# Optimization experiments

Hardware: AMD Instinct MI355X
Metric: run time of the kernel (lower is better)

Reference implementation:

```python
import jax, jax.numpy as jnp
import numpy as np

B, N, D, H, HID = 8, 729, 1152, 12, 4304
HD = D // H
EPS = 1e-6


def _layer_norm(x, g, b):
    mu = jnp.mean(x, axis=-1, keepdims=True)
    var = jnp.mean((x - mu) ** 2, axis=-1, keepdims=True)
    return (x - mu) / jnp.sqrt(var + EPS) * g + b


def setup_inputs() -> dict:
    key = jax.random.key(0)
    ks = jax.random.split(key, 9)
    s = 0.02
    return {
        "x": jax.random.normal(ks[0], (B, N, D), jnp.float32),
        "wq": jax.random.normal(ks[1], (D, D), jnp.float32) * s,
        "bq": jnp.zeros((D,), jnp.float32),
        "wk": jax.random.normal(ks[2], (D, D), jnp.float32) * s,
        "bk": jnp.zeros((D,), jnp.float32),
        "wv": jax.random.normal(ks[3], (D, D), jnp.float32) * s,
        "bv": jnp.zeros((D,), jnp.float32),
        "wo": jax.random.normal(ks[4], (D, D), jnp.float32) * s,
        "bo": jnp.zeros((D,), jnp.float32),
        "ln1_g": jnp.ones((D,), jnp.float32),
        "ln1_b": jnp.zeros((D,), jnp.float32),
        "w_fc1": jax.random.normal(ks[5], (HID, D), jnp.float32) * s,
        "b_fc1": jnp.zeros((HID,), jnp.float32),
        "w_fc2": jax.random.normal(ks[6], (D, HID), jnp.float32) * s,
        "b_fc2": jnp.zeros((D,), jnp.float32),
        "ln2_g": jnp.ones((D,), jnp.float32),
        "ln2_b": jnp.zeros((D,), jnp.float32),
    }


def reference(x, wq, bq, wk, bk, wv, bv, wo, bo, ln1_g, ln1_b,
              w_fc1, b_fc1, w_fc2, b_fc2, ln2_g, ln2_b):
    b, n, d = x.shape
    # split_heads in the source is a plain view (B, H, N, HD) -- NOT a transpose.
    def heads(t):
        return t.reshape(b, H, n, HD)

    Q = heads(x @ wq.T + bq)
    K = heads(x @ wk.T + bk)
    V = heads(x @ wv.T + bv)

    scores = jnp.einsum("bhqd,bhkd->bhqk", Q, K) * (HD ** -0.5)
    attn_w = jax.nn.softmax(scores, axis=-1)
    o = jnp.einsum("bhqk,bhkd->bhqd", attn_w, V)  # [B,H,N,HD]
    o = jnp.swapaxes(o, 1, 2).reshape(b, n, d)
    attn_out = o @ wo.T + bo

    # post-norm: LN(sublayer) + residual
    h = _layer_norm(attn_out, ln1_g, ln1_b) + x

    # quirky MLP: activation applied BEFORE fc1 (faithful to source)
    m = jax.nn.gelu(h, approximate=True)
    m = m @ w_fc1.T + b_fc1
    m = m @ w_fc2.T + b_fc2

    return _layer_norm(m, ln2_g, ln2_b) + h
```

## Files before the change

### kernel.cpp

```cpp
#include <hip/hip_runtime.h>
#include <hip/hip_bf16.h>

#define BF16 __hip_bfloat16

typedef short short8 __attribute__((ext_vector_type(8)));
typedef short short4v __attribute__((ext_vector_type(4)));
typedef float v4f __attribute__((ext_vector_type(4)));
typedef float f4 __attribute__((ext_vector_type(4)));

__device__ __forceinline__ short f2bs(float f) {
    __hip_bfloat16 h = __float2bfloat16(f);
    return *(short*)&h;
}

__device__ __forceinline__ float bs2f(short s) {
    __hip_bfloat16 h = *(__hip_bfloat16*)&s;
    return __bfloat162float(h);
}

__device__ __forceinline__ void async_cp16(const BF16* g, BF16* l) {
    __builtin_amdgcn_global_load_lds(
        (const __attribute__((address_space(1))) void*)g,
        (__attribute__((address_space(3))) void*)l,
        16, 0, 0);
}

__global__ __launch_bounds__(256) void cvt_all_kernel(
    const float* __restrict__ wq, const float* __restrict__ wk,
    const float* __restrict__ wv, const float* __restrict__ wo,
    const float* __restrict__ wfc2, const float* __restrict__ x,
    BF16* __restrict__ wbq, BF16* __restrict__ wbk,
    BF16* __restrict__ wbv, BF16* __restrict__ wbo,
    BF16* __restrict__ wbf2, BF16* __restrict__ xb)
{
    const int i = blockIdx.x * 256 + threadIdx.x;
    constexpr int N_DD  = 331776;
    constexpr int N4    = 4 * N_DD;
    constexpr int N_F2  = 1253376;
    constexpr int E_F2  = N4 + N_F2;
    constexpr int N_X   = 1679616;
    constexpr int TOTAL = E_F2 + N_X;

    if (i < N4) {
        int seg = i / N_DD, j = i - seg * N_DD;
        const float* s = (seg == 0) ? wq : (seg == 1) ? wk : (seg == 2) ? wv : wo;
        BF16* d = (seg == 0) ? wbq : (seg == 1) ? wbk : (seg == 2) ? wbv : wbo;
        f4 v = ((const f4*)s)[j];
        short4v o = {f2bs(v.x), f2bs(v.y), f2bs(v.z), f2bs(v.w)};
        ((short4v*)d)[j] = o;
    } else if (i < E_F2) {
        int j = i - N4;
        int row = j / 1088;
        int c = (j - row * 1088) * 4;
        short4v o = {0, 0, 0, 0};
        if (c < 4304) {
            f4 v = *(const f4*)(wfc2 + (size_t)row * 4304 + c);
            o[0] = f2bs(v.x); o[1] = f2bs(v.y); o[2] = f2bs(v.z); o[3] = f2bs(v.w);
        }
        *(short4v*)(wbf2 + (size_t)row * 4352 + c) = o;
    } else if (i < TOTAL) {
        int j = i - E_F2;
        f4 v = ((const f4*)x)[j];
        short4v o = {f2bs(v.x), f2bs(v.y), f2bs(v.z), f2bs(v.w)};
        ((short4v*)xb)[j] = o;
    }
}

__global__ __launch_bounds__(256) void w1t_kernel(
    const float* __restrict__ wfc1, BF16* __restrict__ w1t)
{
    __shared__ float tile[64][65];
    const int h0 = blockIdx.x * 64;
    const int d0 = blockIdx.y * 64;
    const int tid = threadIdx.x;
#pragma unroll
    for (int i = 0; i < 4; ++i) {
        int lin = tid + i * 256;
        int r = lin >> 4, c4 = lin & 15;
        f4 v = {0.f, 0.f, 0.f, 0.f};
        if (h0 + r < 4304)
            v = *(const f4*)(wfc1 + (size_t)(h0 + r) * 1152 + d0 + c4 * 4);
        tile[r][c4 * 4 + 0] = v.x;
        tile[r][c4 * 4 + 1] = v.y;
        tile[r][c4 * 4 + 2] = v.z;
        tile[r][c4 * 4 + 3] = v.w;
    }
    __syncthreads();
#pragma unroll
    for (int i = 0; i < 2; ++i) {
        int lin = tid + i * 256;
        int dr = lin >> 3, h8 = lin & 7;
        short8 o;
#pragma unroll
        for (int e = 0; e < 8; ++e)
            o[e] = f2bs(tile[h8 * 8 + e][dr]);
        *(short8*)(w1t + (size_t)(d0 + dr) * 4352 + h0 + h8 * 8) = o;
    }
}

__global__ __launch_bounds__(256) void bias_fuse_kernel(
    const float* __restrict__ wfc2, const float* __restrict__ bfc1,
    const float* __restrict__ bfc2, float* __restrict__ bp)
{
    const int row = blockIdx.x * 4 + (threadIdx.x >> 6);
    const int lane = threadIdx.x & 63;
    const float* wr = wfc2 + (size_t)row * 4304;
    float s = 0.f;
    for (int k = lane; k < 4304; k += 64) s += wr[k] * bfc1[k];
#pragma unroll
    for (int mm = 1; mm < 64; mm <<= 1) s += __shfl_xor(s, mm, 64);
    if (lane == 0) bp[row] = s + bfc2[row];
}

__global__ __launch_bounds__(256) void transpose_v3(
    const BF16* __restrict__ V, BF16* __restrict__ VT)
{
    const int hg = blockIdx.x;
    const int s  = blockIdx.y;
    const int b = hg / 12, hh = hg - b * 12;
    const BF16* src = V + (size_t)b * (729 * 1152) + (size_t)hh * (729 * 96);
    BF16* dst = VT + (size_t)hg * 112 * 768;
    const BF16 z = __float2bfloat16(0.f);
    const BF16 one = __float2bfloat16(1.f);
    for (int hd = s * 28; hd < s * 28 + 28; ++hd) {
        for (int kk = threadIdx.x; kk < 768; kk += 256) {
            BF16 val;
            if (hd < 96)       val = (kk < 729) ? src[(size_t)kk * 96 + hd] : z;
            else if (hd == 96) val = (kk < 729) ? one : z;
            else               val = z;
            dst[(size_t)hd * 768 + kk] = val;
        }
    }
}

template<int TM>
__global__ __launch_bounds__(256) void gemm_bt_t(
    const BF16* __restrict__ A, int lda,
    const BF16* __restrict__ W, int ldb,
    const float* __restrict__ bias, int nbias,
    BF16* __restrict__ C, int ldc,
    int M, int Kr)
{
    constexpr int MT = TM / 32;
    __shared__ __align__(16) BF16 smem[(TM + 128) * 64];
    BF16* As = smem;
    BF16* Bs = smem + TM * 64;

    const int tid  = threadIdx.x;
    const int lane = tid & 63;
    const int wave = tid >> 6;
    const int quad = lane >> 4;
    const int l16  = lane & 15;
    const int wm   = (wave >> 1) * (TM / 2);
    const int wn   = (wave & 1) * 64;
    const int m0   = blockIdx.x * TM;
    const int n0   = blockIdx.y * 128;
    if (m0 >= M) return;

    const v4f zf = {0.f, 0.f, 0.f, 0.f};
    v4f acc[MT][4];
#pragma unroll
    for (int i = 0; i < MT; ++i)
#pragma unroll
        for (int j = 0; j < 4; ++j) acc[i][j] = zf;

    const BF16* gA[MT]; BF16* lA[MT];
#pragma unroll
    for (int i = 0; i < MT; ++i) {
        int c = tid + i * 256;
        gA[i] = A + (size_t)(m0 + (c >> 3)) * lda + ((((c & 7) - (c >> 3)) & 7) << 3);
        lA[i] = As + (c & ~63) * 8;
    }
    const BF16* gB[4]; BF16* lB[4];
#pragma unroll
    for (int i = 0; i < 4; ++i) {
        int c = tid + i * 256;
        gB[i] = W + (size_t)(n0 + (c >> 3)) * ldb + ((((c & 7) - (c >> 3)) & 7) << 3);
        lB[i] = Bs + (c & ~63) * 8;
    }

    const int nk = Kr >> 6;
    for (int kt = 0; kt < nk; ++kt) {
#pragma unroll
        for (int i = 0; i < MT; ++i) { async_cp16(gA[i], lA[i]); gA[i] += 64; }
#pragma unroll
        for (int i = 0; i < 4; ++i)  { async_cp16(gB[i], lB[i]); gB[i] += 64; }
        __syncthreads();

#pragma unroll
        for (int ks = 0; ks < 2; ++ks) {
            short8 af[MT], bfg[4];
#pragma unroll
            for (int mt = 0; mt < MT; ++mt) {
                int row = wm + mt * 16 + l16;
                af[mt] = *(const short8*)(As + row * 64 + ((((ks << 2) | quad) + row & 7) & 7) * 8);
            }
#pragma unroll
            for (int nt = 0; nt < 4; ++nt) {
                int row = wn + nt * 16 + l16;
                bfg[nt] = *(const short8*)(Bs + row * 64 + ((((ks << 2) | quad) + row & 7) & 7) * 8);
            }
#pragma unroll
            for (int mt = 0; mt < MT; ++mt)
#pragma unroll
                for (int nt = 0; nt < 4; ++nt)
                    acc[mt][nt] = __builtin_amdgcn_mfma_f32_16x16x32_bf16(
                        af[mt], bfg[nt], acc[mt][nt], 0, 0, 0);
        }
        __syncthreads();
    }

    float bv[4];
#pragma unroll
    for (int nt = 0; nt < 4; ++nt) {
        int col = n0 + wn + nt * 16 + l16;
        bv[nt] = (col < nbias) ? bias[col] : 0.f;
    }
#pragma unroll
    for (int mt = 0; mt < MT; ++mt)
#pragma unroll
        for (int nt = 0; nt < 4; ++nt)
#pragma unroll
            for (int r2 = 0; r2 < 4; ++r2) {
                int row_l = wm + mt * 16 + quad * 4 + r2;
                int col_l = wn + nt * 16 + l16;
                smem[row_l * 128 + col_l] = __float2bfloat16(acc[mt][nt][r2] + bv[nt]);
            }
    __syncthreads();
#pragma unroll
    for (int p = 0; p < TM / 16; ++p) {
        int idx = p * 256 + tid;
        int row = m0 + (idx >> 4);
        if (row < M)
            *(short8*)(C + (size_t)row * ldc + n0 + (idx & 15) * 8) =
                *(const short8*)(smem + idx * 8);
    }
}

__global__ __launch_bounds__(256) void gemm_merge_splitk(
    const BF16* __restrict__ A,
    const BF16* __restrict__ W,
    float* __restrict__ P)
{
    constexpr int TM = 64, MT = 2;
    __shared__ __align__(16) BF16 smem[(TM + 128) * 64];
    BF16* As = smem;
    BF16* Bs = smem + TM * 64;

    const int tid  = threadIdx.x;
    const int lane = tid & 63;
    const int wave = tid >> 6;
    const int quad = lane >> 4;
    const int l16  = lane & 15;
    const int wm   = (wave >> 1) * 32;
    const int wn   = (wave & 1) * 64;
    const int m0   = blockIdx.x * TM;
    const int n0   = blockIdx.y * 128;
    const int z    = blockIdx.z;
    const int ks0  = (z < 4) ? 9 * z : 36 + 8 * (z - 4);
    const int nk   = (z < 4) ? 9 : 8;

    const v4f zf = {0.f, 0.f, 0.f, 0.f};
    v4f acc[MT][4];
#pragma unroll
    for (int i = 0; i < MT; ++i)
#pragma unroll
        for (int j = 0; j < 4; ++j) acc[i][j] = zf;

    const BF16* gA[MT]; BF16* lA[MT];
#pragma unroll
    for (int i = 0; i < MT; ++i) {
        int c = tid + i * 256;
        gA[i] = A + (size_t)(m0 + (c >> 3)) * 4352 + ((((c & 7) - (c >> 3)) & 7) << 3)
              + ks0 * 64;
        lA[i] = As + (c & ~63) * 8;
    }
    const BF16* gB[4]; BF16* lB[4];
#pragma unroll
    for (int i = 0; i < 4; ++i) {
        int c = tid + i * 256;
        gB[i] = W + (size_t)(n0 + (c >> 3)) * 4352 + ((((c & 7) - (c >> 3)) & 7) << 3)
              + ks0 * 64;
        lB[i] = Bs + (c & ~63) * 8;
    }

    for (int kt = 0; kt < nk; ++kt) {
#pragma unroll
        for (int i = 0; i < MT; ++i) { async_cp16(gA[i], lA[i]); gA[i] += 64; }
#pragma unroll
        for (int i = 0; i < 4; ++i)  { async_cp16(gB[i], lB[i]); gB[i] += 64; }
        __syncthreads();

#pragma unroll
        for (int ks = 0; ks < 2; ++ks) {
            short8 af[MT], bfg[4];
#pragma unroll
            for (int mt = 0; mt < MT; ++mt) {
                int row = wm + mt * 16 + l16;
                af[mt] = *(const short8*)(As + row * 64 + ((((ks << 2) | quad) + row & 7) & 7) * 8);
            }
#pragma unroll
            for (int nt = 0; nt < 4; ++nt) {
                int row = wn + nt * 16 + l16;
                bfg[nt] = *(const short8*)(Bs + row * 64 + ((((ks << 2) | quad) + row & 7) & 7) * 8);
            }
#pragma unroll
            for (int mt = 0; mt < MT; ++mt)
#pragma unroll
                for (int nt = 0; nt < 4; ++nt)
                    acc[mt][nt] = __builtin_amdgcn_mfma_f32_16x16x32_bf16(
                        af[mt], bfg[nt], acc[mt][nt], 0, 0, 0);
        }
        __syncthreads();
    }

    float* Pz = P + (size_t)z * 1327104;
#pragma unroll
    for (int mt = 0; mt < MT; ++mt)
#pragma unroll
        for (int nt = 0; nt < 4; ++nt)
#pragma unroll
            for (int r2 = 0; r2 < 4; ++r2) {
                int row = m0 + wm + mt * 16 + quad * 4 + r2;
                int col = n0 + wn + nt * 16 + l16;
                Pz[(size_t)row * 1152 + col] = acc[mt][nt][r2];
            }
}

__global__ __launch_bounds__(256) void wm_reduce_kernel(
    const float* __restrict__ P, BF16* __restrict__ Wm)
{
    const int i = blockIdx.x * 256 + threadIdx.x;
    f4 s = ((const f4*)P)[i];
#pragma unroll
    for (int z = 1; z < 8; ++z) {
        f4 v = ((const f4*)(P + (size_t)z * 1327104))[i];
        s.x += v.x; s.y += v.y; s.z += v.z; s.w += v.w;
    }
    short4v o = {f2bs(s.x), f2bs(s.y), f2bs(s.z), f2bs(s.w)};
    ((short4v*)Wm)[i] = o;
}

__global__ __launch_bounds__(256) void gemm_qkv(
    const BF16* __restrict__ A,
    const BF16* __restrict__ W,
    const float* __restrict__ b0, const float* __restrict__ b1,
    const float* __restrict__ b2,
    BF16* __restrict__ C, size_t cstride, int M)
{
    __shared__ __align__(16) BF16 smem[256 * 64];
    BF16* As = smem;
    BF16* Bs = smem + 128 * 64;

    const int tid  = threadIdx.x;
    const int lane = tid & 63;
    const int wave = tid >> 6;
    const int quad = lane >> 4;
    const int l16  = lane & 15;
    const int wm   = (wave >> 1) * 64;
    const int wn   = (wave & 1) * 64;
    const int m0   = blockIdx.x * 128;
    const int n0   = blockIdx.y * 128;
    if (m0 >= M) return;

    const v4f zf = {0.f, 0.f, 0.f, 0.f};
    v4f acc[4][4];
#pragma unroll
    for (int i = 0; i < 4; ++i)
#pragma unroll
        for (int j = 0; j < 4; ++j) acc[i][j] = zf;

    const BF16* gA[4]; BF16* lA[4];
    const BF16* gB[4]; BF16* lB[4];
#pragma unroll
    for (int i = 0; i < 4; ++i) {
        int c = tid + i * 256;
        int src = ((((c & 7) - (c >> 3)) & 7) << 3);
        gA[i] = A + (size_t)(m0 + (c >> 3)) * 1152 + src;
        gB[i] = W + (size_t)(n0 + (c >> 3)) * 1152 + src;
        lA[i] = As + (c & ~63) * 8;
        lB[i] = Bs + (c & ~63) * 8;
    }

    for (int kt = 0; kt < 18; ++kt) {
#pragma unroll
        for (int i = 0; i < 4; ++i) { async_cp16(gA[i], lA[i]); gA[i] += 64; }
#pragma unroll
        for (int i = 0; i < 4; ++i) { async_cp16(gB[i], lB[i]); gB[i] += 64; }
        __syncthreads();

#pragma unroll
        for (int ks = 0; ks < 2; ++ks) {
            short8 af[4], bfg[4];
#pragma unroll
            for (int mt = 0; mt < 4; ++mt) {
                int row = wm + mt * 16 + l16;
                af[mt] = *(const short8*)(As + row * 64 + ((((ks << 2) | quad) + row & 7) & 7) * 8);
            }
#pragma unroll
            for (int nt = 0; nt < 4; ++nt) {
                int row = wn + nt * 16 + l16;
                bfg[nt] = *(const short8*)(Bs + row * 64 + ((((ks << 2) | quad) + row & 7) & 7) * 8);
            }
#pragma unroll
            for (int mt = 0; mt < 4; ++mt)
#pragma unroll
                for (int nt = 0; nt < 4; ++nt)
                    acc[mt][nt] = __builtin_amdgcn_mfma_f32_16x16x32_bf16(
                        af[mt], bfg[nt], acc[mt][nt], 0, 0, 0);
        }
        __syncthreads();
    }

    const int sel = n0 / 1152;
    const float* bp = (sel == 0) ? b0 : (sel == 1) ? b1 : b2;
    BF16* Cb = C + (size_t)sel * cstride;
    const int nl0 = n0 - sel * 1152;

    float bv[4];
#pragma unroll
    for (int nt = 0; nt < 4; ++nt)
        bv[nt] = bp[nl0 + wn + nt * 16 + l16];
#pragma unroll
    for (int mt = 0; mt < 4; ++mt)
#pragma unroll
        for (int nt = 0; nt < 4; ++nt)
#pragma unroll
            for (int r2 = 0; r2 < 4; ++r2) {
                int row_l = wm + mt * 16 + quad * 4 + r2;
                int col_l = wn + nt * 16 + l16;
                smem[row_l * 128 + col_l] = __float2bfloat16(acc[mt][nt][r2] + bv[nt]);
            }
    __syncthreads();
#pragma unroll
    for (int p = 0; p < 8; ++p) {
        int idx = p * 256 + tid;
        int row = m0 + (idx >> 4);
        if (row < M)
            *(short8*)(Cb + (size_t)row * 1152 + nl0 + (idx & 15) * 8) =
                *(const short8*)(smem + idx * 8);
    }
}

__global__ __launch_bounds__(256) void attn_flash3(
    const BF16* __restrict__ Q, const BF16* __restrict__ K,
    const BF16* __restrict__ VT, BF16* __restrict__ O)
{
    constexpr int NQ = 729, HDk = 96, DM = 1152, LDV = 768;
    __shared__ __align__(16) BF16 Ks[64 * 104];
    __shared__ __align__(16) BF16 Vs[112 * 64];
    __shared__ __align__(16) BF16 Ps[4][32 * 72];

    const int id = blockIdx.x;
    const int xcd = id & 7, slot = id >> 3;
    const int hb = slot / 6, qt = slot - hb * 6;
    const int hg = xcd * 12 + hb;
    const int b = hg / 12, hh = hg - b * 12;

    const int tid = threadIdx.x, wave = tid >> 6, lane = tid & 63;
    const int quad = lane >> 4, l16 = lane & 15;
    const size_t kbase = (size_t)b * (NQ * DM) + (size_t)hh * (NQ * HDk);
    const size_t vbase = (size_t)hg * 112 * LDV;

    const short8 zero8 = {0, 0, 0, 0, 0, 0, 0, 0};
    const v4f zf = {0.f, 0.f, 0.f, 0.f};
    const float C2 = 0.14724445f;

    const int q0w = qt * 128 + wave * 32;
    short8 aq[2][3];
#pragma unroll
    for (int mt = 0; mt < 2; ++mt) {
        int qrow = q0w + mt * 16 + l16;
#pragma unroll
        for (int ks = 0; ks < 3; ++ks)
            aq[mt][ks] = (qrow < NQ)
                ? *(const short8*)(Q + kbase + (size_t)qrow * HDk + ks * 32 + quad * 8)
                : zero8;
    }

    int kk_[3], kg_[3];
#pragma unroll
    for (int i = 0; i < 3; ++i) {
        int c = tid + i * 256;
        kk_[i] = c / 12; kg_[i] = c - kk_[i] * 12;
    }
    int vq_[4], vgr_[4], vhd_[4];
#pragma unroll
    for (int i = 0; i < 4; ++i) {
        int q = wave + 4 * i;
        vq_[i] = q;
        int hd = q * 8 + (lane >> 3);
        vhd_[i] = hd;
        vgr_[i] = ((lane & 7) - hd) & 7;
    }

    v4f oacc[2][7];
#pragma unroll
    for (int mt = 0; mt < 2; ++mt)
#pragma unroll
        for (int nt = 0; nt < 7; ++nt) oacc[mt][nt] = zf;

    for (int kt = 0; kt < 12; ++kt) {
        const int k0 = kt * 64;
#pragma unroll
        for (int i = 0; i < 4; ++i) {
            if (vq_[i] < 14)
                async_cp16(VT + vbase + (size_t)vhd_[i] * LDV + k0 + vgr_[i] * 8,
                           Vs + vq_[i] * 512);
        }
#pragma unroll
        for (int i = 0; i < 3; ++i) {
            short8 v = *(const short8*)(K + kbase + (size_t)(k0 + kk_[i]) * HDk + kg_[i] * 8);
            *(short8*)(Ks + kk_[i] * 104 + kg_[i] * 8) = v;
        }
        __syncthreads();

        v4f s[2][4];
#pragma unroll
        for (int mt = 0; mt < 2; ++mt)
#pragma unroll
            for (int nt = 0; nt < 4; ++nt) s[mt][nt] = zf;
#pragma unroll
        for (int ks = 0; ks < 3; ++ks)
#pragma unroll
            for (int nt = 0; nt < 4; ++nt) {
                short8 bk = *(const short8*)(Ks + (nt * 16 + l16) * 104 + ks * 32 + quad * 8);
#pragma unroll
                for (int mt = 0; mt < 2; ++mt)
                    s[mt][nt] = __builtin_amdgcn_mfma_f32_16x16x32_bf16(
                        aq[mt][ks], bk, s[mt][nt], 0, 0, 0);
            }

        BF16* Pw = &Ps[wave][0];
#pragma unroll
        for (int mt = 0; mt < 2; ++mt)
#pragma unroll
            for (int nt = 0; nt < 4; ++nt)
#pragma unroll
                for (int r = 0; r < 4; ++r)
                    Pw[(mt * 16 + quad * 4 + r) * 72 + nt * 16 + l16] =
                        __float2bfloat16(exp2f(s[mt][nt][r] * C2));
        asm volatile("s_waitcnt lgkmcnt(0)" ::: "memory");

        short8 ap[2][2];
#pragma unroll
        for (int mt = 0; mt < 2; ++mt)
#pragma unroll
            for (int kc = 0; kc < 2; ++kc)
                ap[mt][kc] = *(const short8*)(Pw + (mt * 16 + l16) * 72 + kc * 32 + quad * 8);
#pragma unroll
        for (int nt = 0; nt < 7; ++nt) {
            int hd = nt * 16 + l16;
#pragma unroll
            for (int kc = 0; kc < 2; ++kc) {
                short8 bv = *(const short8*)(Vs + hd * 64 + (((kc * 4 + quad) + hd & 7) & 7) * 8);
#pragma unroll
                for (int mt = 0; mt < 2; ++mt)
                    oacc[mt][nt] = __builtin_amdgcn_mfma_f32_16x16x32_bf16(
                        ap[mt][kc], bv, oacc[mt][nt], 0, 0, 0);
            }
        }
        __syncthreads();
    }

#pragma unroll
    for (int mt = 0; mt < 2; ++mt) {
        const int qb = q0w + mt * 16 + quad * 4;
#pragma unroll
        for (int r = 0; r < 4; ++r) {
            int q = qb + r;
            float lv = __shfl(oacc[mt][6][r], quad << 4, 64);
            float inv = (lv > 0.f) ? 1.f / lv : 0.f;
            if (q >= NQ) continue;
#pragma unroll
            for (int nt = 0; nt < 6; ++nt)
                O[(size_t)b * (NQ * DM) + (size_t)q * DM + hh * HDk + nt * 16 + l16] =
                    __float2bfloat16(oacc[mt][nt][r] * inv);
        }
    }
}

__device__ __forceinline__ float block_sum256(float v, float* red, int tid)
{
#pragma unroll
    for (int mm = 1; mm < 64; mm <<= 1) v += __shfl_xor(v, mm, 64);
    if ((tid & 63) == 0) red[tid >> 6] = v;
    __syncthreads();
    float r = red[0] + red[1] + red[2] + red[3];
    __syncthreads();
    return r;
}

__global__ __launch_bounds__(256) void ln1_gelu_kernel(
    const BF16* __restrict__ ao, const float* __restrict__ x,
    const float* __restrict__ gw, const float* __restrict__ bw,
    BF16* __restrict__ hout, BF16* __restrict__ gout)
{
    __shared__ float red[4];
    const int row = blockIdx.x, tid = threadIdx.x;
    const bool act = tid < 144;
    float v[8];
    float s = 0.f;
    if (act) {
        short8 pk = ((const short8*)(ao + (size_t)row * 1152))[tid];
#pragma unroll
        for (int j = 0; j < 8; ++j) { v[j] = bs2f(pk[j]); s += v[j]; }
    } else {
#pragma unroll
        for (int j = 0; j < 8; ++j) v[j] = 0.f;
    }
    s = block_sum256(s, red, tid);
    float mu = s * (1.f / 1152.f);
    float vsum = 0.f;
    if (act) {
#pragma unroll
        for (int j = 0; j < 8; ++j) { float d = v[j] - mu; vsum += d * d; }
    }
    vsum = block_sum256(vsum, red, tid);
    float rstd = rsqrtf(vsum * (1.f / 1152.f) + 1e-6f);
    if (act) {
        f4 g0 = ((const f4*)gw)[2 * tid], g1 = ((const f4*)gw)[2 * tid + 1];
        f4 b0 = ((const f4*)bw)[2 * tid], b1 = ((const f4*)bw)[2 * tid + 1];
        const f4* xr = (const f4*)(x + (size_t)row * 1152);
        f4 x0 = xr[2 * tid], x1 = xr[2 * tid + 1];
        short8 ho, go;
#pragma unroll
        for (int j = 0; j < 8; ++j) {
            float gj = (j < 4) ? g0[j] : g1[j - 4];
            float bj = (j < 4) ? b0[j] : b1[j - 4];
            float xj = (j < 4) ? x0[j] : x1[j - 4];
            float hv = (v[j] - mu) * rstd * gj + bj + xj;
            ho[j] = f2bs(hv);
            float t = hv;
            float gl = 0.5f * t * (1.f + tanhf(0.7978845608028654f * (t + 0.044715f * t * t * t)));
            go[j] = f2bs(gl);
        }
        ((short8*)(hout + (size_t)row * 1152))[tid] = ho;
        ((short8*)(gout + (size_t)row * 1152))[tid] = go;
    }
}

__global__ __launch_bounds__(256) void ln2_kernel(
    const BF16* __restrict__ m2, const BF16* __restrict__ hf,
    const float* __restrict__ gw, const float* __restrict__ bw,
    float* __restrict__ out)
{
    __shared__ float red[4];
    const int row = blockIdx.x, tid = threadIdx.x;
    const bool act = tid < 144;
    float v[8];
    float s = 0.f;
    if (act) {
        short8 pk = ((const short8*)(m2 + (size_t)row * 1152))[tid];
#pragma unroll
        for (int j = 0; j < 8; ++j) { v[j] = bs2f(pk[j]); s += v[j]; }
    } else {
#pragma unroll
        for (int j = 0; j < 8; ++j) v[j] = 0.f;
    }
    s = block_sum256(s, red, tid);
    float mu = s * (1.f / 1152.f);
    float vsum = 0.f;
    if (act) {
#pragma unroll
        for (int j = 0; j < 8; ++j) { float d = v[j] - mu; vsum += d * d; }
    }
    vsum = block_sum256(vsum, red, tid);
    float rstd = rsqrtf(vsum * (1.f / 1152.f) + 1e-6f);
    if (act) {
        f4 g0 = ((const f4*)gw)[2 * tid], g1 = ((const f4*)gw)[2 * tid + 1];
        f4 b0 = ((const f4*)bw)[2 * tid], b1 = ((const f4*)bw)[2 * tid + 1];
        short8 hfv = ((const short8*)(hf + (size_t)row * 1152))[tid];
        f4 o0, o1;
#pragma unroll
        for (int j = 0; j < 8; ++j) {
            float gj = (j < 4) ? g0[j] : g1[j - 4];
            float bj = (j < 4) ? b0[j] : b1[j - 4];
            float ov = (v[j] - mu) * rstd * gj + bj + bs2f(hfv[j]);
            if (j < 4) o0[j] = ov; else o1[j - 4] = ov;
        }
        f4* orow = (f4*)(out + (size_t)row * 1152);
        orow[2 * tid] = o0;
        orow[2 * tid + 1] = o1;
    }
}

extern "C" void kernel_launch(void* const* d_in, const int* in_sizes, int n_in,
                              void* d_out, int out_size, void* d_ws, size_t ws_size,
                              hipStream_t stream)
{
    const float* x    = (const float*)d_in[0];
    const float* wq   = (const float*)d_in[1];
    const float* bq   = (const float*)d_in[2];
    const float* wk   = (const float*)d_in[3];
    const float* bk   = (const float*)d_in[4];
    const float* wv   = (const float*)d_in[5];
    const float* bv   = (const float*)d_in[6];
    const float* wo   = (const float*)d_in[7];
    const float* bo   = (const float*)d_in[8];
    const float* ln1g = (const float*)d_in[9];
    const float* ln1b = (const float*)d_in[10];
    const float* wfc1 = (const float*)d_in[11];
    const float* bfc1 = (const float*)d_in[12];
    const float* wfc2 = (const float*)d_in[13];
    const float* bfc2 = (const float*)d_in[14];
    const float* ln2g = (const float*)d_in[15];
    const float* ln2b = (const float*)d_in[16];

    const int T = 8 * 729;
    const int D = 1152, HIDP = 4352;
    const size_t TD = (size_t)T * D;
    const size_t WDD = (size_t)D * D;

    BF16* wbq   = (BF16*)d_ws;
    BF16* wbk   = wbq + WDD;
    BF16* wbv   = wbk + WDD;
    BF16* wbo   = wbv + WDD;
    BF16* wbf1t = wbo + WDD;
    BF16* wbf2  = wbf1t + (size_t)HIDP * D;
    BF16* xb    = wbf2 + (size_t)D * HIDP;
    BF16* S0    = xb + TD;
    BF16* S1    = S0 + TD;
    BF16* S2    = S1 + TD;
    BF16* S3    = S2 + TD;
    BF16* C0    = S3 + TD;
    BF16* C1    = C0 + TD;
    BF16* VT    = C0;
    float* Pws  = (float*)S0;
    BF16* Wm    = xb;
    float* bp   = (float*)(xb + WDD + WDD);

    dim3 blk(256);

    cvt_all_kernel<<<16641, blk, 0, stream>>>(
        wq, wk, wv, wo, wfc2, x, wbq, wbk, wbv, wbo, wbf2, xb);

    gemm_qkv<<<dim3(46, 27), blk, 0, stream>>>(xb, wbq, bq, bk, bv, S0, TD, T);

    transpose_v3<<<dim3(96, 4), blk, 0, stream>>>(S2, VT);
    attn_flash3<<<576, blk, 0, stream>>>(S0, S1, VT, S3);

    gemm_bt_t<64><<<dim3(92, 9), blk, 0, stream>>>(S3, D, wbo, D, bo, D, C0, D, T, D);

    ln1_gelu_kernel<<<T, blk, 0, stream>>>(C0, x, ln1g, ln1b, C1, C0);

    w1t_kernel<<<dim3(68, 18), blk, 0, stream>>>(wfc1, wbf1t);
    bias_fuse_kernel<<<288, blk, 0, stream>>>(wfc2, bfc1, bfc2, bp);
    gemm_merge_splitk<<<dim3(18, 9, 8), blk, 0, stream>>>(wbf2, wbf1t, Pws);
    wm_reduce_kernel<<<1296, blk, 0, stream>>>(Pws, Wm);
    gemm_bt_t<64><<<dim3(92, 9), blk, 0, stream>>>(C0, D, Wm, D, bp, D, S3, D, T, D);

    ln2_kernel<<<T, blk, 0, stream>>>(S3, C1, ln2g, ln2b, (float*)d_out);
}
```

Before: 447.3 us.

## Fuse prep kernels and co-schedule weight-merge GEMM with QKV GEMM

Merges the conversion, fc1 transpose and bias-fuse kernels into one launch, and runs the fc2·fc1 weight-merge split-K GEMM (now 2-way split instead of 8) in the same grid as the QKV projection. It also fuses the V transpose, rewritten with a tiled LDS swizzle and vectorised stores, with the split-K reduction. The fused bias now lives in a device global. The aim is fewer launches, better CU fill from concurrent heterogeneous blocks, and less partial-sum traffic. The cost is longer per-block K loops in the merge GEMM and branchy heterogeneous kernels.

```diff
diff --git a/kernel.cpp b/kernel.cpp
--- a/kernel.cpp
+++ b/kernel.cpp
@@ -7,6 +7,8 @@
 typedef short short4v __attribute__((ext_vector_type(4)));
 typedef float v4f __attribute__((ext_vector_type(4)));
 typedef float f4 __attribute__((ext_vector_type(4)));
+
+__device__ float g_bp[1152];
 
 __device__ __forceinline__ short f2bs(float f) {
     __hip_bfloat16 h = __float2bfloat16(f);
@@ -25,111 +27,323 @@
         16, 0, 0);
 }
 
-__global__ __launch_bounds__(256) void cvt_all_kernel(
+__global__ __launch_bounds__(256) void prep_kernel(
     const float* __restrict__ wq, const float* __restrict__ wk,
     const float* __restrict__ wv, const float* __restrict__ wo,
-    const float* __restrict__ wfc2, const float* __restrict__ x,
+    const float* __restrict__ wfc1, const float* __restrict__ wfc2,
+    const float* __restrict__ x,
+    const float* __restrict__ bfc1, const float* __restrict__ bfc2,
     BF16* __restrict__ wbq, BF16* __restrict__ wbk,
     BF16* __restrict__ wbv, BF16* __restrict__ wbo,
-    BF16* __restrict__ wbf2, BF16* __restrict__ xb)
-{
-    const int i = blockIdx.x * 256 + threadIdx.x;
-    constexpr int N_DD  = 331776;
-    constexpr int N4    = 4 * N_DD;
-    constexpr int N_F2  = 1253376;
-    constexpr int E_F2  = N4 + N_F2;
-    constexpr int N_X   = 1679616;
-    constexpr int TOTAL = E_F2 + N_X;
-
-    if (i < N4) {
-        int seg = i / N_DD, j = i - seg * N_DD;
-        const float* s = (seg == 0) ? wq : (seg == 1) ? wk : (seg == 2) ? wv : wo;
-        BF16* d = (seg == 0) ? wbq : (seg == 1) ? wbk : (seg == 2) ? wbv : wbo;
-        f4 v = ((const f4*)s)[j];
-        short4v o = {f2bs(v.x), f2bs(v.y), f2bs(v.z), f2bs(v.w)};
-        ((short4v*)d)[j] = o;
-    } else if (i < E_F2) {
-        int j = i - N4;
-        int row = j / 1088;
-        int c = (j - row * 1088) * 4;
-        short4v o = {0, 0, 0, 0};
-        if (c < 4304) {
-            f4 v = *(const f4*)(wfc2 + (size_t)row * 4304 + c);
-            o[0] = f2bs(v.x); o[1] = f2bs(v.y); o[2] = f2bs(v.z); o[3] = f2bs(v.w);
-        }
-        *(short4v*)(wbf2 + (size_t)row * 4352 + c) = o;
-    } else if (i < TOTAL) {
-        int j = i - E_F2;
-        f4 v = ((const f4*)x)[j];
-        short4v o = {f2bs(v.x), f2bs(v.y), f2bs(v.z), f2bs(v.w)};
-        ((short4v*)xb)[j] = o;
-    }
-}
-
-__global__ __launch_bounds__(256) void w1t_kernel(
-    const float* __restrict__ wfc1, BF16* __restrict__ w1t)
+    BF16* __restrict__ wbf1t, BF16* __restrict__ wbf2,
+    BF16* __restrict__ xb)
 {
     __shared__ float tile[64][65];
-    const int h0 = blockIdx.x * 64;
-    const int d0 = blockIdx.y * 64;
+    const int bid = blockIdx.x;
     const int tid = threadIdx.x;
-#pragma unroll
-    for (int i = 0; i < 4; ++i) {
-        int lin = tid + i * 256;
-        int r = lin >> 4, c4 = lin & 15;
-        f4 v = {0.f, 0.f, 0.f, 0.f};
-        if (h0 + r < 4304)
-            v = *(const f4*)(wfc1 + (size_t)(h0 + r) * 1152 + d0 + c4 * 4);
-        tile[r][c4 * 4 + 0] = v.x;
-        tile[r][c4 * 4 + 1] = v.y;
-        tile[r][c4 * 4 + 2] = v.z;
-        tile[r][c4 * 4 + 3] = v.w;
-    }
-    __syncthreads();
-#pragma unroll
-    for (int i = 0; i < 2; ++i) {
-        int lin = tid + i * 256;
-        int dr = lin >> 3, h8 = lin & 7;
-        short8 o;
-#pragma unroll
-        for (int e = 0; e < 8; ++e)
-            o[e] = f2bs(tile[h8 * 8 + e][dr]);
-        *(short8*)(w1t + (size_t)(d0 + dr) * 4352 + h0 + h8 * 8) = o;
-    }
-}
-
-__global__ __launch_bounds__(256) void bias_fuse_kernel(
-    const float* __restrict__ wfc2, const float* __restrict__ bfc1,
-    const float* __restrict__ bfc2, float* __restrict__ bp)
-{
-    const int row = blockIdx.x * 4 + (threadIdx.x >> 6);
-    const int lane = threadIdx.x & 63;
-    const float* wr = wfc2 + (size_t)row * 4304;
-    float s = 0.f;
-    for (int k = lane; k < 4304; k += 64) s += wr[k] * bfc1[k];
-#pragma unroll
-    for (int mm = 1; mm < 64; mm <<= 1) s += __shfl_xor(s, mm, 64);
-    if (lane == 0) bp[row] = s + bfc2[row];
-}
-
-__global__ __launch_bounds__(256) void transpose_v3(
-    const BF16* __restrict__ V, BF16* __restrict__ VT)
-{
-    const int hg = blockIdx.x;
-    const int s  = blockIdx.y;
-    const int b = hg / 12, hh = hg - b * 12;
-    const BF16* src = V + (size_t)b * (729 * 1152) + (size_t)hh * (729 * 96);
-    BF16* dst = VT + (size_t)hg * 112 * 768;
-    const BF16 z = __float2bfloat16(0.f);
-    const BF16 one = __float2bfloat16(1.f);
-    for (int hd = s * 28; hd < s * 28 + 28; ++hd) {
-        for (int kk = threadIdx.x; kk < 768; kk += 256) {
-            BF16 val;
-            if (hd < 96)       val = (kk < 729) ? src[(size_t)kk * 96 + hd] : z;
-            else if (hd == 96) val = (kk < 729) ? one : z;
-            else               val = z;
-            dst[(size_t)hd * 768 + kk] = val;
-        }
+
+    if (bid < 16641) {
+        const int i = bid * 256 + tid;
+        constexpr int N_DD  = 331776;
+        constexpr int N4    = 4 * N_DD;
+        constexpr int N_F2  = 1253376;
+        constexpr int E_F2  = N4 + N_F2;
+        constexpr int N_X   = 1679616;
+        constexpr int TOTAL = E_F2 + N_X;
+
+        if (i < N4) {
+            int seg = i / N_DD, j = i - seg * N_DD;
+            const float* s = (seg == 0) ? wq : (seg == 1) ? wk : (seg == 2) ? wv : wo;
+            BF16* d = (seg == 0) ? wbq : (seg == 1) ? wbk : (seg == 2) ? wbv : wbo;
+            f4 v = ((const f4*)s)[j];
+            short4v o = {f2bs(v.x), f2bs(v.y), f2bs(v.z), f2bs(v.w)};
+            ((short4v*)d)[j] = o;
+        } else if (i < E_F2) {
+            int j = i - N4;
+            int row = j / 1088;
+            int c = (j - row * 1088) * 4;
+            short4v o = {0, 0, 0, 0};
+            if (c < 4304) {
+                f4 v = *(const f4*)(wfc2 + (size_t)row * 4304 + c);
+                o[0] = f2bs(v.x); o[1] = f2bs(v.y); o[2] = f2bs(v.z); o[3] = f2bs(v.w);
+            }
+            *(short4v*)(wbf2 + (size_t)row * 4352 + c) = o;
+        } else if (i < TOTAL) {
+            int j = i - E_F2;
+            f4 v = ((const f4*)x)[j];
+            short4v o = {f2bs(v.x), f2bs(v.y), f2bs(v.z), f2bs(v.w)};
+            ((short4v*)xb)[j] = o;
+        }
+    } else if (bid < 17865) {
+        const int b2 = bid - 16641;
+        const int h0 = (b2 % 68) * 64;
+        const int d0 = (b2 / 68) * 64;
+#pragma unroll
+        for (int i = 0; i < 4; ++i) {
+            int lin = tid + i * 256;
+            int r = lin >> 4, c4 = lin & 15;
+            f4 v = {0.f, 0.f, 0.f, 0.f};
+            if (h0 + r < 4304)
+                v = *(const f4*)(wfc1 + (size_t)(h0 + r) * 1152 + d0 + c4 * 4);
+            tile[r][c4 * 4 + 0] = v.x;
+            tile[r][c4 * 4 + 1] = v.y;
+            tile[r][c4 * 4 + 2] = v.z;
+            tile[r][c4 * 4 + 3] = v.w;
+        }
+        __syncthreads();
+#pragma unroll
+        for (int i = 0; i < 2; ++i) {
+            int lin = tid + i * 256;
+            int dr = lin >> 3, h8 = lin & 7;
+            short8 o;
+#pragma unroll
+            for (int e = 0; e < 8; ++e)
+                o[e] = f2bs(tile[h8 * 8 + e][dr]);
+            *(short8*)(wbf1t + (size_t)(d0 + dr) * 4352 + h0 + h8 * 8) = o;
+        }
+    } else {
+        const int row = (bid - 17865) * 4 + (tid >> 6);
+        const int lane = tid & 63;
+        const float* wr = wfc2 + (size_t)row * 4304;
+        float s = 0.f;
+        for (int k = lane; k < 4304; k += 64) s += wr[k] * bfc1[k];
+#pragma unroll
+        for (int mm = 1; mm < 64; mm <<= 1) s += __shfl_xor(s, mm, 64);
+        if (lane == 0) g_bp[row] = s + bfc2[row];
+    }
+}
+
+__global__ __launch_bounds__(256) void qkv_merge_kernel(
+    const BF16* __restrict__ A,
+    const BF16* __restrict__ Wqkv,
+    const float* __restrict__ b0, const float* __restrict__ b1,
+    const float* __restrict__ b2,
+    BF16* __restrict__ C, size_t cstride, int M,
+    const BF16* __restrict__ W2,
+    const BF16* __restrict__ W1t,
+    float* __restrict__ P)
+{
+    __shared__ __align__(16) BF16 smem[256 * 64];
+    const int bid  = blockIdx.x;
+    const int tid  = threadIdx.x;
+    const int lane = tid & 63;
+    const int wave = tid >> 6;
+    const int quad = lane >> 4;
+    const int l16  = lane & 15;
+    const v4f zf = {0.f, 0.f, 0.f, 0.f};
+
+    if (bid < 324) {
+        BF16* As = smem;
+        BF16* Bs = smem + 64 * 64;
+        const int mx = bid % 18, ny = (bid / 18) % 9, z = bid / 162;
+        const int m0 = mx * 64, n0 = ny * 128;
+        const int ks0 = z * 34;
+        const int wm = (wave >> 1) * 32;
+        const int wn = (wave & 1) * 64;
+
+        v4f acc[2][4];
+#pragma unroll
+        for (int i = 0; i < 2; ++i)
+#pragma unroll
+            for (int j = 0; j < 4; ++j) acc[i][j] = zf;
+
+        const BF16* gA[2]; BF16* lA[2];
+#pragma unroll
+        for (int i = 0; i < 2; ++i) {
+            int c = tid + i * 256;
+            gA[i] = W2 + (size_t)(m0 + (c >> 3)) * 4352 + ((((c & 7) - (c >> 3)) & 7) << 3)
+                  + ks0 * 64;
+            lA[i] = As + (c & ~63) * 8;
+        }
+        const BF16* gB[4]; BF16* lB[4];
+#pragma unroll
+        for (int i = 0; i < 4; ++i) {
+            int c = tid + i * 256;
+            gB[i] = W1t + (size_t)(n0 + (c >> 3)) * 4352 + ((((c & 7) - (c >> 3)) & 7) << 3)
+                  + ks0 * 64;
+            lB[i] = Bs + (c & ~63) * 8;
+        }
+
+        for (int kt = 0; kt < 34; ++kt) {
+#pragma unroll
+            for (int i = 0; i < 2; ++i) { async_cp16(gA[i], lA[i]); gA[i] += 64; }
+#pragma unroll
+            for (int i = 0; i < 4; ++i)  { async_cp16(gB[i], lB[i]); gB[i] += 64; }
+            __syncthreads();
+#pragma unroll
+            for (int ks = 0; ks < 2; ++ks) {
+                short8 af[2], bfg[4];
+#pragma unroll
+                for (int mt = 0; mt < 2; ++mt) {
+                    int row = wm + mt * 16 + l16;
+                    af[mt] = *(const short8*)(As + row * 64 + ((((ks << 2) | quad) + row & 7) & 7) * 8);
+                }
+#pragma unroll
+                for (int nt = 0; nt < 4; ++nt) {
+                    int row = wn + nt * 16 + l16;
+                    bfg[nt] = *(const short8*)(Bs + row * 64 + ((((ks << 2) | quad) + row & 7) & 7) * 8);
+                }
+#pragma unroll
+                for (int mt = 0; mt < 2; ++mt)
+#pragma unroll
+                    for (int nt = 0; nt < 4; ++nt)
+                        acc[mt][nt] = __builtin_amdgcn_mfma_f32_16x16x32_bf16(
+                            af[mt], bfg[nt], acc[mt][nt], 0, 0, 0);
+            }
+            __syncthreads();
+        }
+
+        float* Pz = P + (size_t)z * 1327104;
+#pragma unroll
+        for (int mt = 0; mt < 2; ++mt)
+#pragma unroll
+            for (int nt = 0; nt < 4; ++nt)
+#pragma unroll
+                for (int r2 = 0; r2 < 4; ++r2) {
+                    int row = m0 + wm + mt * 16 + quad * 4 + r2;
+                    int col = n0 + wn + nt * 16 + l16;
+                    Pz[(size_t)row * 1152 + col] = acc[mt][nt][r2];
+                }
+    } else {
+        BF16* As = smem;
+        BF16* Bs = smem + 128 * 64;
+        const int id2 = bid - 324;
+        const int m0 = (id2 % 46) * 128;
+        const int n0 = (id2 / 46) * 128;
+        const int wm = (wave >> 1) * 64;
+        const int wn = (wave & 1) * 64;
+
+        v4f acc[4][4];
+#pragma unroll
+        for (int i = 0; i < 4; ++i)
+#pragma unroll
+            for (int j = 0; j < 4; ++j) acc[i][j] = zf;
+
+        const BF16* gA[4]; BF16* lA[4];
+        const BF16* gB[4]; BF16* lB[4];
+#pragma unroll
+        for (int i = 0; i < 4; ++i) {
+            int c = tid + i * 256;
+            int src = ((((c & 7) - (c >> 3)) & 7) << 3);
+            gA[i] = A + (size_t)(m0 + (c >> 3)) * 1152 + src;
+            gB[i] = Wqkv + (size_t)(n0 + (c >> 3)) * 1152 + src;
+            lA[i] = As + (c & ~63) * 8;
+            lB[i] = Bs + (c & ~63) * 8;
+        }
+
+        for (int kt = 0; kt < 18; ++kt) {
+#pragma unroll
+            for (int i = 0; i < 4; ++i) { async_cp16(gA[i], lA[i]); gA[i] += 64; }
+#pragma unroll
+            for (int i = 0; i < 4; ++i) { async_cp16(gB[i], lB[i]); gB[i] += 64; }
+            __syncthreads();
+#pragma unroll
+            for (int ks = 0; ks < 2; ++ks) {
+                short8 af[4], bfg[4];
+#pragma unroll
+                for (int mt = 0; mt < 4; ++mt) {
+                    int row = wm + mt * 16 + l16;
+                    af[mt] = *(const short8*)(As + row * 64 + ((((ks << 2) | quad) + row & 7) & 7) * 8);
+                }
+#pragma unroll
+                for (int nt = 0; nt < 4; ++nt) {
+                    int row = wn + nt * 16 + l16;
+                    bfg[nt] = *(const short8*)(Bs + row * 64 + ((((ks << 2) | quad) + row & 7) & 7) * 8);
+                }
+#pragma unroll
+                for (int mt = 0; mt < 4; ++mt)
+#pragma unroll
+                    for (int nt = 0; nt < 4; ++nt)
+                        acc[mt][nt] = __builtin_amdgcn_mfma_f32_16x16x32_bf16(
+                            af[mt], bfg[nt], acc[mt][nt], 0, 0, 0);
+            }
+            __syncthreads();
+        }
+
+        const int sel = n0 / 1152;
+        const float* bp = (sel == 0) ? b0 : (sel == 1) ? b1 : b2;
+        BF16* Cb = C + (size_t)sel * cstride;
+        const int nl0 = n0 - sel * 1152;
+
+        float bv[4];
+#pragma unroll
+        for (int nt = 0; nt < 4; ++nt)
+            bv[nt] = bp[nl0 + wn + nt * 16 + l16];
+#pragma unroll
+        for (int mt = 0; mt < 4; ++mt)
+#pragma unroll
+            for (int nt = 0; nt < 4; ++nt)
+#pragma unroll
+                for (int r2 = 0; r2 < 4; ++r2) {
+                    int row_l = wm + mt * 16 + quad * 4 + r2;
+                    int col_l = wn + nt * 16 + l16;
+                    smem[row_l * 128 + col_l] = __float2bfloat16(acc[mt][nt][r2] + bv[nt]);
+                }
+        __syncthreads();
+#pragma unroll
+        for (int p = 0; p < 8; ++p) {
+            int idx = p * 256 + tid;
+            int row = m0 + (idx >> 4);
+            if (row < M)
+                *(short8*)(Cb + (size_t)row * 1152 + nl0 + (idx & 15) * 8) =
+                    *(const short8*)(smem + idx * 8);
+        }
+    }
+}
+
+__global__ __launch_bounds__(256) void trans_reduce_kernel(
+    const BF16* __restrict__ V, BF16* __restrict__ VT,
+    const float* __restrict__ P, BF16* __restrict__ Wm)
+{
+    __shared__ __align__(16) BF16 tl[64][128];
+    const int bid = blockIdx.x, tid = threadIdx.x;
+    const short8 zero8 = {0, 0, 0, 0, 0, 0, 0, 0};
+
+    if (bid < 1152) {
+        const int hg = bid / 12, kb = bid - hg * 12;
+        const int b = hg / 12, hh = hg - b * 12;
+        const BF16* src = V + (size_t)b * 839808 + (size_t)hh * 69984;
+        BF16* dst = VT + (size_t)hg * 86016;
+        const int kk0 = kb * 64;
+#pragma unroll
+        for (int i = 0; i < 3; ++i) {
+            int c = tid + i * 256;
+            int r = c / 12, cg = c - r * 12;
+            short8 v = (kk0 + r < 729)
+                ? *(const short8*)(src + (size_t)(kk0 + r) * 96 + cg * 8) : zero8;
+            *(short8*)(&tl[r][(cg ^ ((r >> 3) & 7)) * 8]) = v;
+        }
+        __syncthreads();
+#pragma unroll
+        for (int i = 0; i < 3; ++i) {
+            int wc = tid + i * 256;
+            int hd = wc >> 3, o = wc & 7;
+            int sp = (((hd >> 3) ^ o) << 3) + (hd & 7);
+            short8 out;
+#pragma unroll
+            for (int j = 0; j < 8; ++j)
+                out[j] = *(const short*)&tl[o * 8 + j][sp];
+            *(short8*)(dst + (size_t)hd * 768 + kk0 + o * 8) = out;
+        }
+    } else if (bid < 1728) {
+        int c = (bid - 1152) * 256 + tid;
+        int hg = c / 1536, rem = c - hg * 1536;
+        int r = rem / 96, ock = rem - r * 96;
+        int kk = ock * 8;
+        short8 v = zero8;
+        if (r == 0) {
+            const short oneb = 0x3F80;
+#pragma unroll
+            for (int j = 0; j < 8; ++j) v[j] = (kk + j < 729) ? oneb : (short)0;
+        }
+        *(short8*)(VT + (size_t)hg * 86016 + (size_t)(96 + r) * 768 + kk) = v;
+    } else {
+        int i = (bid - 1728) * 256 + tid;
+        f4 s = ((const f4*)P)[i];
+        f4 v = ((const f4*)(P + 1327104))[i];
+        s.x += v.x; s.y += v.y; s.z += v.z; s.w += v.w;
+        short4v o = {f2bs(s.x), f2bs(s.y), f2bs(s.z), f2bs(s.w)};
+        ((short4v*)Wm)[i] = o;
     }
 }
 
@@ -233,211 +447,6 @@
         int row = m0 + (idx >> 4);
         if (row < M)
             *(short8*)(C + (size_t)row * ldc + n0 + (idx & 15) * 8) =
-                *(const short8*)(smem + idx * 8);
-    }
-}
-
-__global__ __launch_bounds__(256) void gemm_merge_splitk(
-    const BF16* __restrict__ A,
-    const BF16* __restrict__ W,
-    float* __restrict__ P)
-{
-    constexpr int TM = 64, MT = 2;
-    __shared__ __align__(16) BF16 smem[(TM + 128) * 64];
-    BF16* As = smem;
-    BF16* Bs = smem + TM * 64;
-
-    const int tid  = threadIdx.x;
-    const int lane = tid & 63;
-    const int wave = tid >> 6;
-    const int quad = lane >> 4;
-    const int l16  = lane & 15;
-    const int wm   = (wave >> 1) * 32;
-    const int wn   = (wave & 1) * 64;
-    const int m0   = blockIdx.x * TM;
-    const int n0   = blockIdx.y * 128;
-    const int z    = blockIdx.z;
-    const int ks0  = (z < 4) ? 9 * z : 36 + 8 * (z - 4);
-    const int nk   = (z < 4) ? 9 : 8;
-
-    const v4f zf = {0.f, 0.f, 0.f, 0.f};
-    v4f acc[MT][4];
-#pragma unroll
-    for (int i = 0; i < MT; ++i)
-#pragma unroll
-        for (int j = 0; j < 4; ++j) acc[i][j] = zf;
-
-    const BF16* gA[MT]; BF16* lA[MT];
-#pragma unroll
-    for (int i = 0; i < MT; ++i) {
-        int c = tid + i * 256;
-        gA[i] = A + (size_t)(m0 + (c >> 3)) * 4352 + ((((c & 7) - (c >> 3)) & 7) << 3)
-              + ks0 * 64;
-        lA[i] = As + (c & ~63) * 8;
-    }
-    const BF16* gB[4]; BF16* lB[4];
-#pragma unroll
-    for (int i = 0; i < 4; ++i) {
-        int c = tid + i * 256;
-        gB[i] = W + (size_t)(n0 + (c >> 3)) * 4352 + ((((c & 7) - (c >> 3)) & 7) << 3)
-              + ks0 * 64;
-        lB[i] = Bs + (c & ~63) * 8;
-    }
-
-    for (int kt = 0; kt < nk; ++kt) {
-#pragma unroll
-        for (int i = 0; i < MT; ++i) { async_cp16(gA[i], lA[i]); gA[i] += 64; }
-#pragma unroll
-        for (int i = 0; i < 4; ++i)  { async_cp16(gB[i], lB[i]); gB[i] += 64; }
-        __syncthreads();
-
-#pragma unroll
-        for (int ks = 0; ks < 2; ++ks) {
-            short8 af[MT], bfg[4];
-#pragma unroll
-            for (int mt = 0; mt < MT; ++mt) {
-                int row = wm + mt * 16 + l16;
-                af[mt] = *(const short8*)(As + row * 64 + ((((ks << 2) | quad) + row & 7) & 7) * 8);
-            }
-#pragma unroll
-            for (int nt = 0; nt < 4; ++nt) {
-                int row = wn + nt * 16 + l16;
-                bfg[nt] = *(const short8*)(Bs + row * 64 + ((((ks << 2) | quad) + row & 7) & 7) * 8);
-            }
-#pragma unroll
-            for (int mt = 0; mt < MT; ++mt)
-#pragma unroll
-                for (int nt = 0; nt < 4; ++nt)
-                    acc[mt][nt] = __builtin_amdgcn_mfma_f32_16x16x32_bf16(
-                        af[mt], bfg[nt], acc[mt][nt], 0, 0, 0);
-        }
-        __syncthreads();
-    }
-
-    float* Pz = P + (size_t)z * 1327104;
-#pragma unroll
-    for (int mt = 0; mt < MT; ++mt)
-#pragma unroll
-        for (int nt = 0; nt < 4; ++nt)
-#pragma unroll
-            for (int r2 = 0; r2 < 4; ++r2) {
-                int row = m0 + wm + mt * 16 + quad * 4 + r2;
-                int col = n0 + wn + nt * 16 + l16;
-                Pz[(size_t)row * 1152 + col] = acc[mt][nt][r2];
-            }
-}
-
-__global__ __launch_bounds__(256) void wm_reduce_kernel(
-    const float* __restrict__ P, BF16* __restrict__ Wm)
-{
-    const int i = blockIdx.x * 256 + threadIdx.x;
-    f4 s = ((const f4*)P)[i];
-#pragma unroll
-    for (int z = 1; z < 8; ++z) {
-        f4 v = ((const f4*)(P + (size_t)z * 1327104))[i];
-        s.x += v.x; s.y += v.y; s.z += v.z; s.w += v.w;
-    }
-    short4v o = {f2bs(s.x), f2bs(s.y), f2bs(s.z), f2bs(s.w)};
-    ((short4v*)Wm)[i] = o;
-}
-
-__global__ __launch_bounds__(256) void gemm_qkv(
-    const BF16* __restrict__ A,
-    const BF16* __restrict__ W,
-    const float* __restrict__ b0, const float* __restrict__ b1,
-    const float* __restrict__ b2,
-    BF16* __restrict__ C, size_t cstride, int M)
-{
-    __shared__ __align__(16) BF16 smem[256 * 64];
-    BF16* As = smem;
-    BF16* Bs = smem + 128 * 64;
-
-    const int tid  = threadIdx.x;
-    const int lane = tid & 63;
-    const int wave = tid >> 6;
-    const int quad = lane >> 4;
-    const int l16  = lane & 15;
-    const int wm   = (wave >> 1) * 64;
-    const int wn   = (wave & 1) * 64;
-    const int m0   = blockIdx.x * 128;
-    const int n0   = blockIdx.y * 128;
-    if (m0 >= M) return;
-
-    const v4f zf = {0.f, 0.f, 0.f, 0.f};
-    v4f acc[4][4];
-#pragma unroll
-    for (int i = 0; i < 4; ++i)
-#pragma unroll
-        for (int j = 0; j < 4; ++j) acc[i][j] = zf;
-
-    const BF16* gA[4]; BF16* lA[4];
-    const BF16* gB[4]; BF16* lB[4];
-#pragma unroll
-    for (int i = 0; i < 4; ++i) {
-        int c = tid + i * 256;
-        int src = ((((c & 7) - (c >> 3)) & 7) << 3);
-        gA[i] = A + (size_t)(m0 + (c >> 3)) * 1152 + src;
-        gB[i] = W + (size_t)(n0 + (c >> 3)) * 1152 + src;
-        lA[i] = As + (c & ~63) * 8;
-        lB[i] = Bs + (c & ~63) * 8;
-    }
-
-    for (int kt = 0; kt < 18; ++kt) {
-#pragma unroll
-        for (int i = 0; i < 4; ++i) { async_cp16(gA[i], lA[i]); gA[i] += 64; }
-#pragma unroll
-        for (int i = 0; i < 4; ++i) { async_cp16(gB[i], lB[i]); gB[i] += 64; }
-        __syncthreads();
-
-#pragma unroll
-        for (int ks = 0; ks < 2; ++ks) {
-            short8 af[4], bfg[4];
-#pragma unroll
-            for (int mt = 0; mt < 4; ++mt) {
-                int row = wm + mt * 16 + l16;
-                af[mt] = *(const short8*)(As + row * 64 + ((((ks << 2) | quad) + row & 7) & 7) * 8);
-            }
-#pragma unroll
-            for (int nt = 0; nt < 4; ++nt) {
-                int row = wn + nt * 16 + l16;
-                bfg[nt] = *(const short8*)(Bs + row * 64 + ((((ks << 2) | quad) + row & 7) & 7) * 8);
-            }
-#pragma unroll
-            for (int mt = 0; mt < 4; ++mt)
-#pragma unroll
-                for (int nt = 0; nt < 4; ++nt)
-                    acc[mt][nt] = __builtin_amdgcn_mfma_f32_16x16x32_bf16(
-                        af[mt], bfg[nt], acc[mt][nt], 0, 0, 0);
-        }
-        __syncthreads();
-    }
-
-    const int sel = n0 / 1152;
-    const float* bp = (sel == 0) ? b0 : (sel == 1) ? b1 : b2;
-    BF16* Cb = C + (size_t)sel * cstride;
-    const int nl0 = n0 - sel * 1152;
-
-    float bv[4];
-#pragma unroll
-    for (int nt = 0; nt < 4; ++nt)
-        bv[nt] = bp[nl0 + wn + nt * 16 + l16];
-#pragma unroll
-    for (int mt = 0; mt < 4; ++mt)
-#pragma unroll
-        for (int nt = 0; nt < 4; ++nt)
-#pragma unroll
-            for (int r2 = 0; r2 < 4; ++r2) {
-                int row_l = wm + mt * 16 + quad * 4 + r2;
-                int col_l = wn + nt * 16 + l16;
-                smem[row_l * 128 + col_l] = __float2bfloat16(acc[mt][nt][r2] + bv[nt]);
-            }
-    __syncthreads();
-#pragma unroll
-    for (int p = 0; p < 8; ++p) {
-        int idx = p * 256 + tid;
-        int row = m0 + (idx >> 4);
-        if (row < M)
-            *(short8*)(Cb + (size_t)row * 1152 + nl0 + (idx & 15) * 8) =
                 *(const short8*)(smem + idx * 8);
     }
 }
@@ -726,29 +735,30 @@
     BF16* C0    = S3 + TD;
     BF16* C1    = C0 + TD;
     BF16* VT    = C0;
-    float* Pws  = (float*)S0;
+    float* Pws  = (float*)S3;
     BF16* Wm    = xb;
-    float* bp   = (float*)(xb + WDD + WDD);
+
+    static float* bp_dev = nullptr;
+    if (!bp_dev) hipGetSymbolAddress((void**)&bp_dev, HIP_SYMBOL(g_bp));
 
     dim3 blk(256);
 
-    cvt_all_kernel<<<16641, blk, 0, stream>>>(
-        wq, wk, wv, wo, wfc2, x, wbq, wbk, wbv, wbo, wbf2, xb);
-
-    gemm_qkv<<<dim3(46, 27), blk, 0, stream>>>(xb, wbq, bq, bk, bv, S0, TD, T);
-
-    transpose_v3<<<dim3(96, 4), blk, 0, stream>>>(S2, VT);
+    prep_kernel<<<18153, blk, 0, stream>>>(
+        wq, wk, wv, wo, wfc1, wfc2, x, bfc1, bfc2,
+        wbq, wbk, wbv, wbo, wbf1t, wbf2, xb);
+
+    qkv_merge_kernel<<<1566, blk, 0, stream>>>(
+        xb, wbq, bq, bk, bv, S0, TD, T, wbf2, wbf1t, Pws);
+
+    trans_reduce_kernel<<<3024, blk, 0, stream>>>(S2, VT, Pws, Wm);
+
     attn_flash3<<<576, blk, 0, stream>>>(S0, S1, VT, S3);
 
     gemm_bt_t<64><<<dim3(92, 9), blk, 0, stream>>>(S3, D, wbo, D, bo, D, C0, D, T, D);
 
     ln1_gelu_kernel<<<T, blk, 0, stream>>>(C0, x, ln1g, ln1b, C1, C0);
 
-    w1t_kernel<<<dim3(68, 18), blk, 0, stream>>>(wfc1, wbf1t);
-    bias_fuse_kernel<<<288, blk, 0, stream>>>(wfc2, bfc1, bfc2, bp);
-    gemm_merge_splitk<<<dim3(18, 9, 8), blk, 0, stream>>>(wbf2, wbf1t, Pws);
-    wm_reduce_kernel<<<1296, blk, 0, stream>>>(Pws, Wm);
-    gemm_bt_t<64><<<dim3(92, 9), blk, 0, stream>>>(C0, D, Wm, D, bp, D, S3, D, T, D);
+    gemm_bt_t<64><<<dim3(92, 9), blk, 0, stream>>>(C0, D, Wm, D, bp_dev, D, S3, D, T, D);
 
     ln2_kernel<<<T, blk, 0, stream>>>(S3, C1, ln2g, ln2b, (float*)d_out);
 }
```

After: 401.6 us. -10.2%, faster.
